# Optimization experiments

Hardware: AMD Instinct MI355X
Metric: run time of the kernel (lower is better)

Reference implementation:

```python
import jax, jax.numpy as jnp
import numpy as np

B, H, L, N2 = 8, 256, 4096, 32  # N2 = d_state // 2 (conjugate-pair parameterization)


def _s4d_kernel(log_dt, log_A_real, A_imag, C_re, C_im, length):
    """S4D (diag) SSM convolution kernel via ZOH discretization. Returns (H, L) real."""
    dt = jnp.exp(log_dt)                               # (H,)
    A = -jnp.exp(log_A_real) + 1j * A_imag             # (H, N2) complex, Re<0
    C = C_re + 1j * C_im                               # (H, N2)
    dtA = A * dt[:, None]                              # (H, N2)
    # Vandermonde matrix exp(dtA * l), l = 0..L-1 : (H, N2, L)
    V = jnp.exp(dtA[:, :, None] * jnp.arange(length, dtype=log_dt.dtype))
    Ck = C * (jnp.exp(dtA) - 1.0) / A                  # absorb ZOH B-scaling into C
    # factor 2 accounts for the implicit conjugate pairs
    return 2.0 * jnp.einsum('hn,hnl->hl', Ck, V).real


def setup_inputs() -> dict:
    key = jax.random.key(0)
    ks = jax.random.split(key, 8)
    hidden_states = jax.random.normal(ks[0], (B, H, L), dtype=jnp.float32)
    # dt log-uniform in [1e-3, 1e-1]
    log_dt = jnp.log(1e-3) + jax.random.uniform(ks[1], (H,), dtype=jnp.float32) * (
        jnp.log(1e-1) - jnp.log(1e-3))
    # diag-lin init: A = -1/2 + i*pi*n
    log_A_real = jnp.log(0.5 * jnp.ones((H, N2), dtype=jnp.float32))
    A_imag = jnp.broadcast_to(np.pi * jnp.arange(N2, dtype=jnp.float32), (H, N2)).copy()
    C_re = jax.random.normal(ks[2], (H, N2), dtype=jnp.float32) * (0.5 ** 0.5)
    C_im = jax.random.normal(ks[3], (H, N2), dtype=jnp.float32) * (0.5 ** 0.5)
    D = jax.random.normal(ks[4], (H,), dtype=jnp.float32)
    # output position-wise linear H -> 2H followed by GLU
    W_out = jax.random.normal(ks[5], (2 * H, H), dtype=jnp.float32) * (1.0 / np.sqrt(H))
    b_out = jnp.zeros((2 * H,), dtype=jnp.float32)
    return {"hidden_states": hidden_states, "log_dt": log_dt, "log_A_real": log_A_real,
            "A_imag": A_imag, "C_re": C_re, "C_im": C_im, "D": D,
            "W_out": W_out, "b_out": b_out}


def reference(hidden_states, log_dt, log_A_real, A_imag, C_re, C_im, D, W_out, b_out):
    _, _, length = hidden_states.shape
    k = _s4d_kernel(log_dt, log_A_real, A_imag, C_re, C_im, length)  # (H, L)
    n_fft = 2 * length
    k_f = jnp.fft.rfft(k, n=n_fft)                     # (H, L+1)
    u_f = jnp.fft.rfft(hidden_states, n=n_fft)         # (B, H, L+1)
    y = jnp.fft.irfft(u_f * k_f, n=n_fft)[..., :length]  # causal long conv
    y = y + hidden_states * D[:, None]                 # skip connection
    y = jax.nn.gelu(y, approximate=False)              # torch F.gelu (exact erf)
    y = jnp.einsum('oh,bhl->bol', W_out, y) + b_out[None, :, None]  # (B, 2H, L)
    a, g = jnp.split(y, 2, axis=1)                     # GLU
    return a * jax.nn.sigmoid(g)                       # (B, H, L)
```

## Files before the change

kernel.cpp:

```cpp
#include <hip/hip_runtime.h>
#include <hip/hip_bf16.h>

#define B_   8
#define H_   256
#define L_   4096
#define N2_  32

typedef __attribute__((ext_vector_type(8))) short bf16x8;
typedef __attribute__((ext_vector_type(4))) float f32x4;

__device__ __forceinline__ unsigned short f2bf(float x) {
    __hip_bfloat16 h = __float2bfloat16(x);
    unsigned short us;
    __builtin_memcpy(&us, &h, 2);
    return us;
}

union BF8 { ushort4 u4[2]; unsigned short s[8]; bf16x8 v; };

__device__ __forceinline__ float gelu_exact(float y) {
    return 0.5f * y * (1.0f + erff(y * 0.70710678118654752440f));
}

__device__ __forceinline__ void fast_sincos(float x, float* s, float* c) {
    float rev = x * 0.15915494309189535f;
    rev = rev - floorf(rev);
    *s = __builtin_amdgcn_sinf(rev);
    *c = __builtin_amdgcn_cosf(rev);
}

__global__ __launch_bounds__(256) void prep_kernel(
    const float* __restrict__ log_dt,
    const float* __restrict__ log_A_real,
    const float* __restrict__ A_imag,
    const float* __restrict__ C_re,
    const float* __restrict__ C_im,
    const float* __restrict__ Dp,
    const float* __restrict__ W,
    unsigned short* __restrict__ MAT,
    unsigned short* __restrict__ W2)
{
    const int bid = blockIdx.x;
    const int tid = threadIdx.x;
    if (bid >= 256) {
        int gq = (bid - 256) * 256 + tid;
        int m = gq >> 6, t = gq & 63;
        int ks = t >> 4, sub = t & 15;
        int gr = sub >> 1, e4 = (sub & 1) * 4;
        int klog = ks * 64 + ((gr ^ (m & 7)) << 3) + e4;
        float4 wv = *(const float4*)&W[m * 256 + klog];
        ushort4 o;
        o.x = f2bf(wv.x); o.y = f2bf(wv.y); o.z = f2bf(wv.z); o.w = f2bf(wv.w);
        *(ushort4*)&W2[ks * 32768 + m * 64 + gr * 8 + e4] = o;
        return;
    }
    const int h    = bid;
    const int j    = tid & 63;
    const int part = tid >> 6;

    __shared__ float sAr[32], sAi[32], sK2r[32], sK2i[32];
    __shared__ float sTap[4][64];
    __shared__ unsigned short sQ[64 * 68];

    unsigned short* __restrict__ Pd  = MAT + (size_t)h * 12288;
    unsigned short* __restrict__ Tkd = Pd + 4096;
    unsigned short* __restrict__ Qd  = Pd + 8192;
    const float dt = __expf(log_dt[h]);

    if (tid < 32) {
        int n = tid;
        float Ar = -__expf(log_A_real[h * 32 + n]);
        float Ai = A_imag[h * 32 + n];
        float er = __expf(dt * Ar);
        float s, c; fast_sincos(dt * Ai, &s, &c);
        float wr = er * c, wi = er * s;
        float Cr = C_re[h * 32 + n], Ci = C_im[h * 32 + n];
        float den = Ar * Ar + Ai * Ai;
        float nr = wr - 1.0f, ni = wi;
        float qr = (nr * Ar + ni * Ai) / den;
        float qi = (ni * Ar - nr * Ai) / den;
        sAr[n] = Ar; sAi[n] = Ai;
        sK2r[n] = 2.0f * (Cr * qr - Ci * qi);
        sK2i[n] = 2.0f * (Cr * qi + Ci * qr);
    }
    __syncthreads();

    {
        float pdt = dt * (float)(63 - j);
        #pragma unroll
        for (int q = 0; q < 8; ++q) {
            int n = part * 8 + q;
            float mag = __expf(pdt * sAr[n]);
            float s, c; fast_sincos(pdt * sAi[n], &s, &c);
            Pd[(2 * n)     * 64 + j] = f2bf(mag * c);
            Pd[(2 * n + 1) * 64 + j] = f2bf(mag * s);
        }
    }
    {
        float jdt = dt * (float)j;
        float acc = 0.0f;
        #pragma unroll
        for (int q = 0; q < 8; ++q) {
            int n = part * 8 + q;
            float mag = __expf(jdt * sAr[n]);
            float s, c; fast_sincos(jdt * sAi[n], &s, &c);
            acc = fmaf(sK2r[n], mag * c, fmaf(-sK2i[n], mag * s, acc));
        }
        sTap[part][j] = acc;
        float j1dt = dt * (float)(j + 1);
        #pragma unroll
        for (int q = 0; q < 8; ++q) {
            int n = part * 8 + q;
            float mag = __expf(j1dt * sAr[n]);
            float s, c; fast_sincos(j1dt * sAi[n], &s, &c);
            float wpr = mag * c, wpi = mag * s;
            sQ[j * 68 + 2 * n]     = f2bf(sK2r[n] * wpr - sK2i[n] * wpi);
            sQ[j * 68 + 2 * n + 1] = f2bf(-(sK2r[n] * wpi + sK2i[n] * wpr));
        }
    }
    __syncthreads();
    if (part == 0) {
        float v = sTap[0][j] + sTap[1][j] + sTap[2][j] + sTap[3][j];
        if (j == 0) v += Dp[h];
        sTap[0][j] = v;
    }
    __syncthreads();

    {
        int r  = tid >> 2;
        int c0 = (tid & 3) * 16;
        #pragma unroll
        for (int cc = 0; cc < 16; cc += 4) {
            int c = c0 + cc;
            ushort4 v;
            v.x = (r - c     >= 0) ? f2bf(sTap[0][r - c])     : (unsigned short)0;
            v.y = (r - c - 1 >= 0) ? f2bf(sTap[0][r - c - 1]) : (unsigned short)0;
            v.z = (r - c - 2 >= 0) ? f2bf(sTap[0][r - c - 2]) : (unsigned short)0;
            v.w = (r - c - 3 >= 0) ? f2bf(sTap[0][r - c - 3]) : (unsigned short)0;
            *(ushort4*)&Tkd[r * 64 + c] = v;
        }
    }
    #pragma unroll
    for (int it = 0; it < 4; ++it) {
        int quad = it * 256 + tid;
        int row = quad >> 4, c4 = (quad & 15) * 4;
        ushort4 v;
        v.x = sQ[row * 68 + c4];     v.y = sQ[row * 68 + c4 + 1];
        v.z = sQ[row * 68 + c4 + 2]; v.w = sQ[row * 68 + c4 + 3];
        *(ushort4*)&Qd[row * 64 + c4] = v;
    }
}

__global__ __launch_bounds__(256, 2) void s4_mfma_kernel(
    const float* __restrict__ u,
    const float* __restrict__ log_dt,
    const float* __restrict__ log_A_real,
    const float* __restrict__ A_imag,
    const unsigned short* __restrict__ MAT,
    unsigned short* __restrict__ Gout)
{
    __shared__ __align__(16) unsigned char smem[4 * 17408];
    const int tid  = threadIdx.x;
    const int w    = tid >> 6;
    const int lane = tid & 63;
    const int ln15 = lane & 15;
    const int hi4  = (lane >> 4) * 4;
    const int hi8  = (lane >> 4) * 8;
    const int bid  = blockIdx.x;
    const int b    = bid >> 6, hg = bid & 63;
    const int h    = hg * 4 + w;

    float* Eb = (float*)(smem + w * 17408);
    unsigned short* yb = (unsigned short*)(smem + w * 17408);

    const float* __restrict__ urow = u + ((size_t)(b * H_ + h)) * L_;
    const unsigned short* __restrict__ Ph  = MAT + (size_t)h * 12288;
    const unsigned short* __restrict__ Tkh = Ph + 4096;
    const unsigned short* __restrict__ Qh  = Ph + 8192;

    float wTr, wTi;
    {
        int n = lane & 31;
        float dt = expf(log_dt[h]);
        float Ar = -expf(log_A_real[h * 32 + n]);
        float Ai = A_imag[h * 32 + n];
        float er = expf(dt * Ar); float s, c; sincosf(dt * Ai, &s, &c);
        float pr = er * c, pi = er * s;
        #pragma unroll
        for (int k = 0; k < 6; ++k) { float a2 = pr*pr - pi*pi, b2 = 2.0f*pr*pi; pr = a2; pi = b2; }
        wTr = pr; wTi = pi;
    }

    bf16x8 ufr[4][2];
    #pragma unroll
    for (int nt = 0; nt < 4; ++nt) {
        int c = nt * 16 + ln15;
        #pragma unroll
        for (int ks = 0; ks < 2; ++ks) {
            const float* p = urow + c * 64 + ks * 32 + hi8;
            float4 lo = *(const float4*)p;
            float4 hi = *(const float4*)(p + 4);
            BF8 t8;
            t8.s[0]=f2bf(lo.x); t8.s[1]=f2bf(lo.y); t8.s[2]=f2bf(lo.z); t8.s[3]=f2bf(lo.w);
            t8.s[4]=f2bf(hi.x); t8.s[5]=f2bf(hi.y); t8.s[6]=f2bf(hi.z); t8.s[7]=f2bf(hi.w);
            ufr[nt][ks] = t8.v;
        }
    }
    #pragma unroll
    for (int mt = 0; mt < 4; ++mt) {
        bf16x8 pa[2];
        #pragma unroll
        for (int ks = 0; ks < 2; ++ks)
            pa[ks] = *(const bf16x8*)&Ph[(mt * 16 + ln15) * 64 + ks * 32 + hi8];
        f32x4 e[4];
        #pragma unroll
        for (int nt = 0; nt < 4; ++nt) e[nt] = (f32x4){0.f, 0.f, 0.f, 0.f};
        #pragma unroll
        for (int ks = 0; ks < 2; ++ks)
            #pragma unroll
            for (int nt = 0; nt < 4; ++nt)
                e[nt] = __builtin_amdgcn_mfma_f32_16x16x32_bf16(pa[ks], ufr[nt][ks], e[nt], 0, 0, 0);
        #pragma unroll
        for (int nt = 0; nt < 4; ++nt)
            *(f32x4*)&Eb[(nt * 16 + ln15) * 68 + mt * 16 + hi4] = e[nt];
    }
    __syncthreads();

    if (lane < 32) {
        int n2 = 2 * lane;
        float Xr = 0.0f, Xi = 0.0f;
        float2 e = *(float2*)&Eb[n2];
        #pragma unroll 4
        for (int c = 0; c < 64; ++c) {
            float2 en = e;
            if (c < 63) en = *(float2*)&Eb[(c + 1) * 68 + n2];
            *(float2*)&Eb[c * 68 + n2] = make_float2(Xr, Xi);
            float nXr = fmaf(wTr, Xr, fmaf(-wTi, Xi, e.x));
            float nXi = fmaf(wTi, Xr, fmaf( wTr, Xi, e.y));
            Xr = nXr; Xi = nXi; e = en;
        }
    }
    __syncthreads();

    bf16x8 sfr[4][2];
    #pragma unroll
    for (int nt = 0; nt < 4; ++nt) {
        int c = nt * 16 + ln15;
        #pragma unroll
        for (int ks = 0; ks < 2; ++ks) {
            float4 lo = *(const float4*)&Eb[c * 68 + ks * 32 + hi8];
            float4 hi = *(const float4*)&Eb[c * 68 + ks * 32 + hi8 + 4];
            BF8 t8;
            t8.s[0]=f2bf(lo.x); t8.s[1]=f2bf(lo.y); t8.s[2]=f2bf(lo.z); t8.s[3]=f2bf(lo.w);
            t8.s[4]=f2bf(hi.x); t8.s[5]=f2bf(hi.y); t8.s[6]=f2bf(hi.z); t8.s[7]=f2bf(hi.w);
            sfr[nt][ks] = t8.v;
        }
    }
    #pragma unroll
    for (int mt = 0; mt < 4; ++mt) {
        bf16x8 ta[2], qa[2];
        #pragma unroll
        for (int ks = 0; ks < 2; ++ks) {
            ta[ks] = *(const bf16x8*)&Tkh[(mt * 16 + ln15) * 64 + ks * 32 + hi8];
            qa[ks] = *(const bf16x8*)&Qh [(mt * 16 + ln15) * 64 + ks * 32 + hi8];
        }
        #pragma unroll
        for (int nt = 0; nt < 4; ++nt) {
            f32x4 a = (f32x4){0.f, 0.f, 0.f, 0.f};
            #pragma unroll
            for (int ks = 0; ks < 2; ++ks) {
                a = __builtin_amdgcn_mfma_f32_16x16x32_bf16(ta[ks], ufr[nt][ks], a, 0, 0, 0);
                a = __builtin_amdgcn_mfma_f32_16x16x32_bf16(qa[ks], sfr[nt][ks], a, 0, 0, 0);
            }
            int c  = nt * 16 + ln15;
            int j0 = mt * 16 + hi4;
            ushort4 o;
            o.x = f2bf(gelu_exact(a[0]));
            o.y = f2bf(gelu_exact(a[1]));
            o.z = f2bf(gelu_exact(a[2]));
            o.w = f2bf(gelu_exact(a[3]));
            *(ushort4*)&yb[c * 68 + j0] = o;
        }
    }
    __syncthreads();

    unsigned short* __restrict__ Grow = Gout + ((size_t)(b * 64 + hg)) * (L_ * 4);
    #pragma unroll
    for (int it = 0; it < 16; ++it) {
        int l = it * 256 + tid;
        int c = l >> 6, j = l & 63;
        ushort4 pk;
        pk.x = ((unsigned short*)(smem + 0 * 17408))[c * 68 + j];
        pk.y = ((unsigned short*)(smem + 1 * 17408))[c * 68 + j];
        pk.z = ((unsigned short*)(smem + 2 * 17408))[c * 68 + j];
        pk.w = ((unsigned short*)(smem + 3 * 17408))[c * 68 + j];
        *(ushort4*)&Grow[(size_t)l * 4] = pk;
    }
}

__global__ __launch_bounds__(256, 3) void glu_gemm_kernel(
    const unsigned short* __restrict__ G,
    const unsigned short* __restrict__ W2,
    const float* __restrict__ bo,
    float* __restrict__ out)
{
    __shared__ __align__(16) unsigned char smem[36864];
    unsigned short* sW = (unsigned short*)smem;

    const int tid  = threadIdx.x;
    const int lane = tid & 63;
    const int wv   = tid >> 6;
    const int wm   = wv >> 1;
    const int wn   = wv & 1;
    const int ln15 = lane & 15;
    const int hi   = lane >> 4;

    const int l0 = blockIdx.x * 64;
    const int m0 = blockIdx.y * 128;
    const int b  = blockIdx.z;
    const int col0 = l0 + wn * 32 + ln15;

    f32x4 acc[8][2];
    #pragma unroll
    for (int i = 0; i < 8; ++i)
        #pragma unroll
        for (int j = 0; j < 2; ++j) acc[i][j] = (f32x4){0.f, 0.f, 0.f, 0.f};

    BF8 bb[4][2];
    auto loadB = [&](int ksub, BF8* dst) {
        int hg0 = ksub * 8 + hi * 2;
        size_t base = ((size_t)(b * 64 + hg0) * 4096 + col0) * 4;
        dst[0].u4[0] = *(const ushort4*)&G[base];
        dst[0].u4[1] = *(const ushort4*)&G[base + 16384];
        dst[1].u4[0] = *(const ushort4*)&G[base + 64];
        dst[1].u4[1] = *(const ushort4*)&G[base + 16384 + 64];
    };
    #pragma unroll
    for (int p = 0; p < 4; ++p) loadB(p, bb[p]);

    #pragma unroll
    for (int ksub = 0; ksub < 8; ++ksub) {
        if ((ksub & 1) == 0) {
            const int ks = ksub >> 1;
            __syncthreads();
            const unsigned short* src1 = W2 + (size_t)ks * 32768 + m0 * 64;
            const unsigned short* src2 = W2 + (size_t)ks * 32768 + (256 + m0) * 64;
            uint4 t[8];
            #pragma unroll
            for (int i = 0; i < 4; ++i) t[i]     = *(const uint4*)&src1[i * 2048 + tid * 8];
            #pragma unroll
            for (int i = 0; i < 4; ++i) t[4 + i] = *(const uint4*)&src2[i * 2048 + tid * 8];
            #pragma unroll
            for (int i = 0; i < 8; ++i)
                *(uint4*)&sW[i * 2048 + tid * 8] = t[i];
            __syncthreads();
        }
        const int slot = ksub & 3;
        const int gl = (ksub & 1) * 4 + hi;
        #pragma unroll
        for (int half = 0; half < 2; ++half) {
            bf16x8 af[4];
            #pragma unroll
            for (int mt = 0; mt < 4; ++mt) {
                int r = half * 128 + wm * 64 + mt * 16 + ln15;
                af[mt] = *(const bf16x8*)((const unsigned char*)sW + r * 128 + ((gl ^ (r & 7)) << 4));
            }
            #pragma unroll
            for (int mt = 0; mt < 4; ++mt)
                #pragma unroll
                for (int nb = 0; nb < 2; ++nb)
                    acc[half * 4 + mt][nb] =
                        __builtin_amdgcn_mfma_f32_16x16x32_bf16(af[mt], bb[slot][nb].v,
                                                                acc[half * 4 + mt][nb], 0, 0, 0);
        }
        if (ksub < 4) loadB(ksub + 4, bb[slot]);
    }

    __syncthreads();
    float* sEp = (float*)smem + wv * 2304;
    #pragma unroll
    for (int mt = 0; mt < 4; ++mt) {
        int r0 = mt * 16 + hi * 4;
        float4 ba = *(const float4*)&bo[m0 + wm * 64 + r0];
        float4 bg = *(const float4*)&bo[256 + m0 + wm * 64 + r0];
        #pragma unroll
        for (int nb = 0; nb < 2; ++nb) {
            #pragma unroll
            for (int rr = 0; rr < 4; ++rr) {
                float a = acc[mt][nb][rr]     + ((const float*)&ba)[rr];
                float g = acc[4 + mt][nb][rr] + ((const float*)&bg)[rr];
                sEp[(r0 + rr) * 36 + nb * 16 + ln15] = a / (1.0f + __expf(-g));
            }
        }
    }
    __syncthreads();
    {
        const int rl = lane >> 3;
        const int c4 = (lane & 7) * 4;
        float* obase = out + ((size_t)(b * 256 + m0 + wm * 64)) * 4096 + l0 + wn * 32;
        #pragma unroll
        for (int ps = 0; ps < 8; ++ps) {
            int row = ps * 8 + rl;
            float4 v = *(const float4*)&sEp[row * 36 + c4];
            *(float4*)&obase[(size_t)row * 4096 + c4] = v;
        }
    }
}

extern "C" void kernel_launch(void* const* d_in, const int* in_sizes, int n_in,
                              void* d_out, int out_size, void* d_ws, size_t ws_size,
                              hipStream_t stream) {
    (void)in_sizes; (void)n_in; (void)out_size;
    const float* hs     = (const float*)d_in[0];
    const float* log_dt = (const float*)d_in[1];
    const float* logA   = (const float*)d_in[2];
    const float* Aim    = (const float*)d_in[3];
    const float* Cre    = (const float*)d_in[4];
    const float* Cim    = (const float*)d_in[5];
    const float* Dp     = (const float*)d_in[6];
    const float* Wout   = (const float*)d_in[7];
    const float* bout   = (const float*)d_in[8];
    float* out          = (float*)d_out;

    unsigned short* G   = (unsigned short*)d_ws;
    unsigned short* MAT = (unsigned short*)((char*)d_ws + 16777216);
    unsigned short* W2  = (unsigned short*)((char*)d_ws + 23068672);

    if (ws_size < (size_t)23330816) return;

    prep_kernel<<<dim3(384), dim3(256), 0, stream>>>(
        log_dt, logA, Aim, Cre, Cim, Dp, Wout, MAT, W2);
    s4_mfma_kernel<<<dim3(512), dim3(256), 0, stream>>>(
        hs, log_dt, logA, Aim, MAT, G);
    glu_gemm_kernel<<<dim3(64, 2, 8), dim3(256), 0, stream>>>(
        G, W2, bout, out);
}
```

Measured before the change: 54.89 us.

## Store SSM intermediate state as bf16 in LDS to raise occupancy

The s4 kernel now keeps the per-wave E/state buffer in bf16 instead of fp32, which roughly halves LDS per block and raises the launch bounds target from 2 to 4 blocks per CU. The scan loop reads packed bf16 pairs and writes bf16 states, and the second MFMA stage loads bf16x8 fragments directly without converting. The GLU epilogue is also reorganized so each block stores rows of 64 contiguous floats rather than per-wave 32-wide segments. Rounding E to bf16 before the recurrence adds precision loss in the scan inputs, and the tighter register budget may cause spills.

```diff
diff --git a/kernel.cpp b/kernel.cpp
--- a/kernel.cpp
+++ b/kernel.cpp
@@ -151,7 +151,7 @@
     }
 }
 
-__global__ __launch_bounds__(256, 2) void s4_mfma_kernel(
+__global__ __launch_bounds__(256, 4) void s4_mfma_kernel(
     const float* __restrict__ u,
     const float* __restrict__ log_dt,
     const float* __restrict__ log_A_real,
@@ -159,7 +159,7 @@
     const unsigned short* __restrict__ MAT,
     unsigned short* __restrict__ Gout)
 {
-    __shared__ __align__(16) unsigned char smem[4 * 17408];
+    __shared__ __align__(16) unsigned short smem[4 * 64 * 72];
     const int tid  = threadIdx.x;
     const int w    = tid >> 6;
     const int lane = tid & 63;
@@ -170,8 +170,7 @@
     const int b    = bid >> 6, hg = bid & 63;
     const int h    = hg * 4 + w;
 
-    float* Eb = (float*)(smem + w * 17408);
-    unsigned short* yb = (unsigned short*)(smem + w * 17408);
+    unsigned short* Ew = smem + w * 4608;
 
     const float* __restrict__ urow = u + ((size_t)(b * H_ + h)) * L_;
     const unsigned short* __restrict__ Ph  = MAT + (size_t)h * 12288;
@@ -221,23 +220,30 @@
             for (int nt = 0; nt < 4; ++nt)
                 e[nt] = __builtin_amdgcn_mfma_f32_16x16x32_bf16(pa[ks], ufr[nt][ks], e[nt], 0, 0, 0);
         #pragma unroll
-        for (int nt = 0; nt < 4; ++nt)
-            *(f32x4*)&Eb[(nt * 16 + ln15) * 68 + mt * 16 + hi4] = e[nt];
+        for (int nt = 0; nt < 4; ++nt) {
+            ushort4 pk;
+            pk.x = f2bf(e[nt][0]); pk.y = f2bf(e[nt][1]);
+            pk.z = f2bf(e[nt][2]); pk.w = f2bf(e[nt][3]);
+            *(ushort4*)&Ew[(nt * 16 + ln15) * 72 + mt * 16 + hi4] = pk;
+        }
     }
     __syncthreads();
 
     if (lane < 32) {
-        int n2 = 2 * lane;
+        const int n2 = 2 * lane;
         float Xr = 0.0f, Xi = 0.0f;
-        float2 e = *(float2*)&Eb[n2];
+        unsigned int eu = *(const unsigned int*)&Ew[n2];
         #pragma unroll 4
         for (int c = 0; c < 64; ++c) {
-            float2 en = e;
-            if (c < 63) en = *(float2*)&Eb[(c + 1) * 68 + n2];
-            *(float2*)&Eb[c * 68 + n2] = make_float2(Xr, Xi);
-            float nXr = fmaf(wTr, Xr, fmaf(-wTi, Xi, e.x));
-            float nXi = fmaf(wTi, Xr, fmaf( wTr, Xi, e.y));
-            Xr = nXr; Xi = nXi; e = en;
+            unsigned int en = eu;
+            if (c < 63) en = *(const unsigned int*)&Ew[(c + 1) * 72 + n2];
+            float er = __uint_as_float(eu << 16);
+            float ei = __uint_as_float(eu & 0xffff0000u);
+            *(unsigned int*)&Ew[c * 72 + n2] =
+                (unsigned int)f2bf(Xr) | ((unsigned int)f2bf(Xi) << 16);
+            float nXr = fmaf(wTr, Xr, fmaf(-wTi, Xi, er));
+            float nXi = fmaf(wTi, Xr, fmaf( wTr, Xi, ei));
+            Xr = nXr; Xi = nXi; eu = en;
         }
     }
     __syncthreads();
@@ -247,14 +253,8 @@
     for (int nt = 0; nt < 4; ++nt) {
         int c = nt * 16 + ln15;
         #pragma unroll
-        for (int ks = 0; ks < 2; ++ks) {
-            float4 lo = *(const float4*)&Eb[c * 68 + ks * 32 + hi8];
-            float4 hi = *(const float4*)&Eb[c * 68 + ks * 32 + hi8 + 4];
-            BF8 t8;
-            t8.s[0]=f2bf(lo.x); t8.s[1]=f2bf(lo.y); t8.s[2]=f2bf(lo.z); t8.s[3]=f2bf(lo.w);
-            t8.s[4]=f2bf(hi.x); t8.s[5]=f2bf(hi.y); t8.s[6]=f2bf(hi.z); t8.s[7]=f2bf(hi.w);
-            sfr[nt][ks] = t8.v;
-        }
+        for (int ks = 0; ks < 2; ++ks)
+            sfr[nt][ks] = *(const bf16x8*)&Ew[c * 72 + ks * 32 + hi8];
     }
     #pragma unroll
     for (int mt = 0; mt < 4; ++mt) {
@@ -279,7 +279,7 @@
             o.y = f2bf(gelu_exact(a[1]));
             o.z = f2bf(gelu_exact(a[2]));
             o.w = f2bf(gelu_exact(a[3]));
-            *(ushort4*)&yb[c * 68 + j0] = o;
+            *(ushort4*)&Ew[c * 72 + j0] = o;
         }
     }
     __syncthreads();
@@ -290,10 +290,10 @@
         int l = it * 256 + tid;
         int c = l >> 6, j = l & 63;
         ushort4 pk;
-        pk.x = ((unsigned short*)(smem + 0 * 17408))[c * 68 + j];
-        pk.y = ((unsigned short*)(smem + 1 * 17408))[c * 68 + j];
-        pk.z = ((unsigned short*)(smem + 2 * 17408))[c * 68 + j];
-        pk.w = ((unsigned short*)(smem + 3 * 17408))[c * 68 + j];
+        pk.x = smem[0 * 4608 + c * 72 + j];
+        pk.y = smem[1 * 4608 + c * 72 + j];
+        pk.z = smem[2 * 4608 + c * 72 + j];
+        pk.w = smem[3 * 4608 + c * 72 + j];
         *(ushort4*)&Grow[(size_t)l * 4] = pk;
     }
 }
@@ -377,32 +377,31 @@
     }
 
     __syncthreads();
-    float* sEp = (float*)smem + wv * 2304;
+    float* sGlu = (float*)smem;
     #pragma unroll
     for (int mt = 0; mt < 4; ++mt) {
-        int r0 = mt * 16 + hi * 4;
-        float4 ba = *(const float4*)&bo[m0 + wm * 64 + r0];
-        float4 bg = *(const float4*)&bo[256 + m0 + wm * 64 + r0];
+        int r0 = wm * 64 + mt * 16 + hi * 4;
+        float4 ba = *(const float4*)&bo[m0 + r0];
+        float4 bg = *(const float4*)&bo[256 + m0 + r0];
         #pragma unroll
         for (int nb = 0; nb < 2; ++nb) {
             #pragma unroll
             for (int rr = 0; rr < 4; ++rr) {
                 float a = acc[mt][nb][rr]     + ((const float*)&ba)[rr];
                 float g = acc[4 + mt][nb][rr] + ((const float*)&bg)[rr];
-                sEp[(r0 + rr) * 36 + nb * 16 + ln15] = a / (1.0f + __expf(-g));
+                sGlu[(r0 + rr) * 68 + wn * 32 + nb * 16 + ln15] = a / (1.0f + __expf(-g));
             }
         }
     }
     __syncthreads();
     {
-        const int rl = lane >> 3;
-        const int c4 = (lane & 7) * 4;
-        float* obase = out + ((size_t)(b * 256 + m0 + wm * 64)) * 4096 + l0 + wn * 32;
-        #pragma unroll
-        for (int ps = 0; ps < 8; ++ps) {
-            int row = ps * 8 + rl;
-            float4 v = *(const float4*)&sEp[row * 36 + c4];
-            *(float4*)&obase[(size_t)row * 4096 + c4] = v;
+        const int rloc = tid >> 4;
+        const int c4   = (tid & 15) * 4;
+        #pragma unroll
+        for (int it2 = 0; it2 < 8; ++it2) {
+            int row = it2 * 16 + rloc;
+            float4 v = *(const float4*)&sGlu[row * 68 + c4];
+            *(float4*)&out[((size_t)(b * 256 + m0 + row)) * 4096 + l0 + c4] = v;
         }
     }
 }
```

Result: slower. 57.18 us (+4.2%).
